# Kernel optimization log

Hardware: AMD Instinct MI355X
Metric: run time of the kernel (lower is better)

Reference implementation:

```python
import jax, jax.numpy as jnp
import numpy as np

N_EMB = 1024
EMB_DIM = 256
BETA = 10.0


def setup_inputs() -> dict:
    key = jax.random.key(0)
    k1, k2 = jax.random.split(key)
    z = jax.random.normal(k1, (64, 32, 32, EMB_DIM), dtype=jnp.float32)
    # torch init: uniform(-1/n_embeddings, 1/n_embeddings)
    codebook = jax.random.uniform(k2, (N_EMB, EMB_DIM), dtype=jnp.float32,
                                  minval=-1.0 / N_EMB, maxval=1.0 / N_EMB)
    return {"z": z, "codebook": codebook}


def reference(z, codebook):
    beta = BETA
    d_model = z.shape[-1]
    z_flat = z.reshape(-1, d_model)  # [T, D]
    # squared euclidean distances: ||z||^2 + ||e||^2 - 2 z e^T  -> [T, N]
    d = (jnp.sum(z_flat ** 2, axis=1, keepdims=True)
         + jnp.sum(codebook ** 2, axis=1)
         - 2.0 * jnp.matmul(z_flat, codebook.T))
    indices = jnp.argmin(d, axis=-1).reshape(z.shape[:-1])  # [B, H, W]
    z_q = codebook[indices]  # [B, H, W, D]
    loss = (jnp.mean((jax.lax.stop_gradient(z_q) - z) ** 2)
            + beta * jnp.mean((z_q - jax.lax.stop_gradient(z)) ** 2))
    # straight-through estimator
    z_q = z + jax.lax.stop_gradient(z_q - z)
    return (z_q, loss, indices)
```

## Files before the change

kernel.cpp:

```cpp
#include <hip/hip_runtime.h>
#include <math.h>


#define NTOK     65536
#define DDIM     256
#define NCODE    1024
#define LOSS_OFF 16777216
#define IDX_OFF  16777217


__global__ void vq_prep(const float* __restrict__ cb, float* __restrict__ wsB,
                        double* __restrict__ loss_acc,
                        unsigned long long* __restrict__ keys)
{
#pragma clang fp contract(off)
    int gid = blockIdx.x * blockDim.x + threadIdx.x;
    if (gid == 0) *loss_acc = 0.0;
    unsigned long long* kp = keys + (size_t)gid * 4;
    kp[0] = kp[1] = kp[2] = kp[3] = 0xFFFFFFFFFFFFFFFFull;
    if (gid >= NCODE) return;
    const float* a = cb + gid * DDIM;
    float half[2];
    for (int h = 0; h < 2; ++h) {
        const float* b = a + h * 128;
        float r[8];
#pragma unroll
        for (int j = 0; j < 8; ++j) { float v = b[j]; r[j] = v * v; }
        for (int i = 8; i < 128; i += 8) {
#pragma unroll
            for (int j = 0; j < 8; ++j) { float v = b[i + j]; float s = v * v; r[j] = r[j] + s; }
        }
        half[h] = ((r[0] + r[1]) + (r[2] + r[3])) + ((r[4] + r[5]) + (r[6] + r[7]));
    }
    wsB[gid] = half[0] + half[1];
}

__global__ void vq_anorm(const float* __restrict__ z, float* __restrict__ wsA)
{
#pragma clang fp contract(off)
    int t = blockIdx.x * blockDim.x + threadIdx.x;
    const float* a = z + (size_t)t * DDIM;
    float half[2];
    for (int h = 0; h < 2; ++h) {
        const float* b = a + h * 128;
        float r[8];
#pragma unroll
        for (int j = 0; j < 8; ++j) { float v = b[j]; r[j] = v * v; }
        for (int i = 8; i < 128; i += 8) {
#pragma unroll
            for (int j = 0; j < 8; ++j) { float v = b[i + j]; float s = v * v; r[j] = r[j] + s; }
        }
        half[h] = ((r[0] + r[1]) + (r[2] + r[3])) + ((r[4] + r[5]) + (r[6] + r[7]));
    }
    wsA[t] = half[0] + half[1];
}

__global__ __launch_bounds__(512) void vq_main(const float* __restrict__ z,
                                               const float* __restrict__ cb,
                                               const float* __restrict__ wsB,
                                               const float* __restrict__ wsA,
                                               unsigned long long* __restrict__ keys)
{
    __shared__ float zs[32][128];
    __shared__ float es[32][128];
    __shared__ float Bl[128];

    const int tid = threadIdx.x;
    const int tx = tid & 15, ty = tid >> 4;
    const int b = blockIdx.x;
    const int xcd = b & 7, sl = b >> 3;
    const int tt = xcd * 64 + (sl >> 3);
    const int ct = sl & 7;
    const int t0 = tt * 128;
    const int n0 = ct * 128;

    if (tid < 128) Bl[tid] = wsB[n0 + tid];

    float4 Av4 = *(const float4*)(wsA + t0 + 4 * ty);
    float Aval[4] = {Av4.x, Av4.y, Av4.z, Av4.w};

    float acc[4][8];
#pragma unroll
    for (int i = 0; i < 4; ++i)
#pragma unroll
        for (int j = 0; j < 8; ++j) acc[i][j] = 0.0f;

    float4 zr[2], er[2];

#define STAGE_LOAD(kc_)                                                           \
    {                                                                             \
        const float* zb_ = z  + (size_t)t0 * DDIM + (kc_) * 32;                   \
        const float* eb_ = cb + (size_t)n0 * DDIM + (kc_) * 32;                   \
        _Pragma("unroll")                                                         \
        for (int s_ = 0; s_ < 2; ++s_) {                                          \
            int g_ = tid + 512 * s_; int row_ = g_ >> 3; int c4_ = g_ & 7;        \
            zr[s_] = *(const float4*)(zb_ + row_ * DDIM + c4_ * 4);               \
            er[s_] = *(const float4*)(eb_ + row_ * DDIM + c4_ * 4);               \
        }                                                                         \
    }

    STAGE_LOAD(0);

    for (int kc = 0; kc < 8; ++kc) {
        __syncthreads();
#pragma unroll
        for (int s_ = 0; s_ < 2; ++s_) {
            int g = tid + 512 * s_; int row = g >> 3; int c4 = g & 7;
            int p = row ^ ((c4 & 3) << 3);
            zs[c4 * 4 + 0][p] = zr[s_].x; zs[c4 * 4 + 1][p] = zr[s_].y;
            zs[c4 * 4 + 2][p] = zr[s_].z; zs[c4 * 4 + 3][p] = zr[s_].w;
            es[c4 * 4 + 0][p] = er[s_].x; es[c4 * 4 + 1][p] = er[s_].y;
            es[c4 * 4 + 2][p] = er[s_].z; es[c4 * 4 + 3][p] = er[s_].w;
        }
        __syncthreads();
        if (kc < 7) STAGE_LOAD(kc + 1);

#pragma unroll
        for (int k = 0; k < 32; ++k) {
            int cx = ((k >> 2) & 3) << 1;
            float4 a0 = *(const float4*)&zs[k][4 * (ty ^ cx)];
            float4 b0 = *(const float4*)&es[k][4 * (tx ^ cx)];
            float4 b1 = *(const float4*)&es[k][64 + 4 * (tx ^ cx)];
            float za[4] = {a0.x, a0.y, a0.z, a0.w};
            float eb[8] = {b0.x, b0.y, b0.z, b0.w, b1.x, b1.y, b1.z, b1.w};
#pragma unroll
            for (int i = 0; i < 4; ++i)
#pragma unroll
                for (int j = 0; j < 8; ++j)
                    acc[i][j] = __builtin_fmaf(za[i], eb[j], acc[i][j]);
        }
    }

    float best[4];
    int   bidx[4];
#pragma unroll
    for (int i = 0; i < 4; ++i) { best[i] = __builtin_inff(); bidx[i] = 0x7fffffff; }
#pragma unroll
    for (int i = 0; i < 4; ++i)
#pragma unroll
        for (int j = 0; j < 8; ++j) {
            int cl = (j < 4) ? (4 * tx + j) : (64 + 4 * tx + (j - 4));
            float t1 = Aval[i] + Bl[cl];
            float dist = t1 - 2.0f * acc[i][j];
            if (dist < best[i]) { best[i] = dist; bidx[i] = n0 + cl; }
        }

#pragma unroll
    for (int i = 0; i < 4; ++i) {
        float d = best[i]; int w = bidx[i];
        for (int off = 8; off; off >>= 1) {
            float od = __shfl_xor(d, off);
            int   ow = __shfl_xor(w, off);
            if (od < d || (od == d && ow < w)) { d = od; w = ow; }
        }
        best[i] = d; bidx[i] = w;
    }

    if (tx == 0) {
#pragma unroll
        for (int i = 0; i < 4; ++i) {
            unsigned long long key =
                ((unsigned long long)__float_as_uint(best[i]) << 32) |
                (unsigned int)bidx[i];
            atomicMin(&keys[t0 + 4 * ty + i], key);
        }
    }
#undef STAGE_LOAD
}

__global__ __launch_bounds__(256) void vq_gather(const float* __restrict__ z,
                                                 const float* __restrict__ cb,
                                                 const unsigned long long* __restrict__ keys,
                                                 double* __restrict__ loss_acc,
                                                 float* __restrict__ out)
{
    __shared__ double lred[4];
    const int tid = threadIdx.x;
    const int tx = tid & 15, ty = tid >> 4;
    const int t0 = blockIdx.x * 64;

    double ld = 0.0;
#pragma unroll
    for (int i = 0; i < 4; ++i) {
        int t = t0 + ty * 4 + i;
        unsigned long long key = keys[t];
        int w = (int)(unsigned int)(key & 0xFFFFFFFFull);
        const float4* crow = (const float4*)(cb + (size_t)w * DDIM);
        const float4* zrow = (const float4*)(z + (size_t)t * DDIM);
        float4* orow = (float4*)(out + (size_t)t * DDIM);
#pragma unroll
        for (int q = 0; q < 4; ++q) {
            int c4 = tx * 4 + q;
            float4 e4 = crow[c4];
            float4 z4 = zrow[c4];
            float4 o;
            float dx;
            dx = e4.x - z4.x; o.x = z4.x + dx; ld += (double)(dx * dx);
            dx = e4.y - z4.y; o.y = z4.y + dx; ld += (double)(dx * dx);
            dx = e4.z - z4.z; o.z = z4.z + dx; ld += (double)(dx * dx);
            dx = e4.w - z4.w; o.w = z4.w + dx; ld += (double)(dx * dx);
            orow[c4] = o;
        }
        if (tx == 0) out[IDX_OFF + t] = (float)w;
    }

    for (int off = 32; off; off >>= 1) ld += __shfl_down(ld, off);
    int lane = tid & 63, wv = tid >> 6;
    if (lane == 0) lred[wv] = ld;
    __syncthreads();
    if (tid == 0) {
        double s = (lred[0] + lred[1]) + (lred[2] + lred[3]);
        atomicAdd(loss_acc, s);
    }
}

__global__ void vq_finish(const double* __restrict__ loss_acc, float* __restrict__ out)
{
#pragma clang fp contract(off)
    double m = *loss_acc / 16777216.0;
    float mf = (float)m;
    float second = 10.0f * mf;
    out[LOSS_OFF] = mf + second;
}

extern "C" void kernel_launch(void* const* d_in, const int* in_sizes, int n_in,
                              void* d_out, int out_size, void* d_ws, size_t ws_size,
                              hipStream_t stream)
{
    (void)in_sizes; (void)n_in; (void)out_size; (void)ws_size;
    const float* z  = (const float*)d_in[0];
    const float* cb = (const float*)d_in[1];
    float* out = (float*)d_out;
    double* loss_acc = (double*)d_ws;
    float* wsB = (float*)((char*)d_ws + 64);
    unsigned long long* keys = (unsigned long long*)((char*)d_ws + 8192);
    float* wsA = (float*)((char*)d_ws + 532480);

    vq_prep<<<dim3(64), dim3(256), 0, stream>>>(cb, wsB, loss_acc, keys);
    vq_anorm<<<dim3(NTOK / 256), dim3(256), 0, stream>>>(z, wsA);
    vq_main<<<dim3(4096), dim3(512), 0, stream>>>(z, cb, wsB, wsA, keys);
    vq_gather<<<dim3(NTOK / 64), dim3(256), 0, stream>>>(z, cb, keys, loss_acc, out);
    vq_finish<<<dim3(1), dim3(1), 0, stream>>>(loss_acc, out);
}
```

Measured before the change: 463.1 us.

## Restructure VQ distance kernel: wave-uniform z loads, async LDS codebook double-buffer

Reworks the main distance kernel so each wave owns 16 tokens and each lane owns two codes. The z rows are read straight from global memory with wave-uniform addresses (broadcast loads), so z no longer goes through LDS. Codebook tiles are double-buffered in LDS using global_load_lds async copies, and each token's argmin is reduced with a full-wave shuffle. This is meant to cut LDS traffic and barriers and to overlap loads with compute. The risk is that uniform global z loads become latency-bound and the per-token 64-lane shuffle reductions add overhead.

```diff
diff --git a/kernel.cpp b/kernel.cpp
--- a/kernel.cpp
+++ b/kernel.cpp
@@ -8,6 +8,11 @@
 #define LOSS_OFF 16777216
 #define IDX_OFF  16777217
 
+
+#define GLOAD_LDS16(gp, lp)                                                       \
+    __builtin_amdgcn_global_load_lds(                                             \
+        (const __attribute__((address_space(1))) void*)(gp),                      \
+        (__attribute__((address_space(3))) void*)(lp), 16, 0, 0)
 
 __global__ void vq_prep(const float* __restrict__ cb, float* __restrict__ wsB,
                         double* __restrict__ loss_acc,
@@ -61,12 +66,11 @@
                                                const float* __restrict__ wsA,
                                                unsigned long long* __restrict__ keys)
 {
-    __shared__ float zs[32][128];
-    __shared__ float es[32][128];
-    __shared__ float Bl[128];
+    __shared__ float es[2][128 * 32];
 
     const int tid = threadIdx.x;
-    const int tx = tid & 15, ty = tid >> 4;
+    const int L = tid & 63;
+    const int wv = __builtin_amdgcn_readfirstlane(tid >> 6);
     const int b = blockIdx.x;
     const int xcd = b & 7, sl = b >> 3;
     const int tt = xcd * 64 + (sl >> 3);
@@ -74,98 +78,73 @@
     const int t0 = tt * 128;
     const int n0 = ct * 128;
 
-    if (tid < 128) Bl[tid] = wsB[n0 + tid];
-
-    float4 Av4 = *(const float4*)(wsA + t0 + 4 * ty);
-    float Aval[4] = {Av4.x, Av4.y, Av4.z, Av4.w};
-
-    float acc[4][8];
-#pragma unroll
-    for (int i = 0; i < 4; ++i)
-#pragma unroll
-        for (int j = 0; j < 8; ++j) acc[i][j] = 0.0f;
-
-    float4 zr[2], er[2];
-
-#define STAGE_LOAD(kc_)                                                           \
-    {                                                                             \
-        const float* zb_ = z  + (size_t)t0 * DDIM + (kc_) * 32;                   \
-        const float* eb_ = cb + (size_t)n0 * DDIM + (kc_) * 32;                   \
-        _Pragma("unroll")                                                         \
-        for (int s_ = 0; s_ < 2; ++s_) {                                          \
-            int g_ = tid + 512 * s_; int row_ = g_ >> 3; int c4_ = g_ & 7;        \
-            zr[s_] = *(const float4*)(zb_ + row_ * DDIM + c4_ * 4);               \
-            er[s_] = *(const float4*)(eb_ + row_ * DDIM + c4_ * 4);               \
-        }                                                                         \
-    }
-
-    STAGE_LOAD(0);
-
+    const float* zw = z + (size_t)(t0 + 16 * wv) * DDIM;
+
+    const float B0 = wsB[n0 + L];
+    const float B1 = wsB[n0 + 64 + L];
+
+    const char* cbc = (const char*)cb;
+    const long eoffA = (long)(n0 + wv * 8 + (L >> 3)) * 1024 + (L & 7) * 16;
+    const long eoffB = (long)(n0 + 64 + wv * 8 + (L >> 3)) * 1024 + (L & 7) * 16;
+
+    float acc[16][2];
+#pragma unroll
+    for (int i = 0; i < 16; ++i) { acc[i][0] = 0.0f; acc[i][1] = 0.0f; }
+
+    GLOAD_LDS16(cbc + eoffA, &es[0][wv * 256]);
+    GLOAD_LDS16(cbc + eoffB, &es[0][2048 + wv * 256]);
+    __syncthreads();
+
+    int cur = 0;
     for (int kc = 0; kc < 8; ++kc) {
+        if (kc < 7) {
+            GLOAD_LDS16(cbc + eoffA + (kc + 1) * 128, &es[cur ^ 1][wv * 256]);
+            GLOAD_LDS16(cbc + eoffB + (kc + 1) * 128, &es[cur ^ 1][2048 + wv * 256]);
+        }
+        const float* ep0 = &es[cur][32 * L];
+        const float* ep1 = &es[cur][2048 + 32 * L];
+#pragma unroll
+        for (int ks = 0; ks < 8; ++ks) {
+            float4 ea = *(const float4*)(ep0 + 4 * ks);
+            float4 eb = *(const float4*)(ep1 + 4 * ks);
+            const float* zk = zw + (kc * 8 + ks) * 4;
+#pragma unroll
+            for (int tok = 0; tok < 16; ++tok) {
+                float4 zf = *(const float4*)(zk + tok * 256);
+                acc[tok][0] = __builtin_fmaf(zf.x, ea.x, acc[tok][0]);
+                acc[tok][0] = __builtin_fmaf(zf.y, ea.y, acc[tok][0]);
+                acc[tok][0] = __builtin_fmaf(zf.z, ea.z, acc[tok][0]);
+                acc[tok][0] = __builtin_fmaf(zf.w, ea.w, acc[tok][0]);
+                acc[tok][1] = __builtin_fmaf(zf.x, eb.x, acc[tok][1]);
+                acc[tok][1] = __builtin_fmaf(zf.y, eb.y, acc[tok][1]);
+                acc[tok][1] = __builtin_fmaf(zf.z, eb.z, acc[tok][1]);
+                acc[tok][1] = __builtin_fmaf(zf.w, eb.w, acc[tok][1]);
+            }
+        }
         __syncthreads();
-#pragma unroll
-        for (int s_ = 0; s_ < 2; ++s_) {
-            int g = tid + 512 * s_; int row = g >> 3; int c4 = g & 7;
-            int p = row ^ ((c4 & 3) << 3);
-            zs[c4 * 4 + 0][p] = zr[s_].x; zs[c4 * 4 + 1][p] = zr[s_].y;
-            zs[c4 * 4 + 2][p] = zr[s_].z; zs[c4 * 4 + 3][p] = zr[s_].w;
-            es[c4 * 4 + 0][p] = er[s_].x; es[c4 * 4 + 1][p] = er[s_].y;
-            es[c4 * 4 + 2][p] = er[s_].z; es[c4 * 4 + 3][p] = er[s_].w;
-        }
-        __syncthreads();
-        if (kc < 7) STAGE_LOAD(kc + 1);
-
-#pragma unroll
-        for (int k = 0; k < 32; ++k) {
-            int cx = ((k >> 2) & 3) << 1;
-            float4 a0 = *(const float4*)&zs[k][4 * (ty ^ cx)];
-            float4 b0 = *(const float4*)&es[k][4 * (tx ^ cx)];
-            float4 b1 = *(const float4*)&es[k][64 + 4 * (tx ^ cx)];
-            float za[4] = {a0.x, a0.y, a0.z, a0.w};
-            float eb[8] = {b0.x, b0.y, b0.z, b0.w, b1.x, b1.y, b1.z, b1.w};
-#pragma unroll
-            for (int i = 0; i < 4; ++i)
-#pragma unroll
-                for (int j = 0; j < 8; ++j)
-                    acc[i][j] = __builtin_fmaf(za[i], eb[j], acc[i][j]);
-        }
-    }
-
-    float best[4];
-    int   bidx[4];
-#pragma unroll
-    for (int i = 0; i < 4; ++i) { best[i] = __builtin_inff(); bidx[i] = 0x7fffffff; }
-#pragma unroll
-    for (int i = 0; i < 4; ++i)
-#pragma unroll
-        for (int j = 0; j < 8; ++j) {
-            int cl = (j < 4) ? (4 * tx + j) : (64 + 4 * tx + (j - 4));
-            float t1 = Aval[i] + Bl[cl];
-            float dist = t1 - 2.0f * acc[i][j];
-            if (dist < best[i]) { best[i] = dist; bidx[i] = n0 + cl; }
-        }
-
-#pragma unroll
-    for (int i = 0; i < 4; ++i) {
-        float d = best[i]; int w = bidx[i];
-        for (int off = 8; off; off >>= 1) {
+        cur ^= 1;
+    }
+
+    unsigned long long mykey = 0xFFFFFFFFFFFFFFFFull;
+#pragma unroll
+    for (int tok = 0; tok < 16; ++tok) {
+        float A = wsA[t0 + 16 * wv + tok];
+        float t1a = A + B0;
+        float dA = t1a - 2.0f * acc[tok][0];
+        float t1b = A + B1;
+        float dB = t1b - 2.0f * acc[tok][1];
+        float d; int n;
+        if (dB < dA) { d = dB; n = n0 + 64 + L; }
+        else         { d = dA; n = n0 + L; }
+        for (int off = 1; off < 64; off <<= 1) {
             float od = __shfl_xor(d, off);
-            int   ow = __shfl_xor(w, off);
-            if (od < d || (od == d && ow < w)) { d = od; w = ow; }
-        }
-        best[i] = d; bidx[i] = w;
-    }
-
-    if (tx == 0) {
-#pragma unroll
-        for (int i = 0; i < 4; ++i) {
-            unsigned long long key =
-                ((unsigned long long)__float_as_uint(best[i]) << 32) |
-                (unsigned int)bidx[i];
-            atomicMin(&keys[t0 + 4 * ty + i], key);
-        }
-    }
-#undef STAGE_LOAD
+            int   on = __shfl_xor(n, off);
+            if (od < d || (od == d && on < n)) { d = od; n = on; }
+        }
+        if (L == tok) mykey = ((unsigned long long)__float_as_uint(d) << 32) |
+                              (unsigned int)n;
+    }
+    if (L < 16) atomicMin(&keys[t0 + 16 * wv + L], mykey);
 }
 
 __global__ __launch_bounds__(256) void vq_gather(const float* __restrict__ z,
@@ -205,8 +184,8 @@
     }
 
     for (int off = 32; off; off >>= 1) ld += __shfl_down(ld, off);
-    int lane = tid & 63, wv = tid >> 6;
-    if (lane == 0) lred[wv] = ld;
+    int lane = tid & 63, wvv = tid >> 6;
+    if (lane == 0) lred[wvv] = ld;
     __syncthreads();
     if (tid == 0) {
         double s = (lred[0] + lred[1]) + (lred[2] + lred[3]);
```

Result: slower. 1.383 ms (+198.6%).
